# Optimization experiments

Measured on AMD Instinct MI355X. Metric: run time of the kernel, lower is better.

## Reference

```python
import jax, jax.numpy as jnp
import numpy as np
import math

B, Q, K, C, H, D = 4, 2048, 2048, 128, 8, 16  # c_q=c_k=c_v=C, c_hidden=D, no_heads=H


def setup_inputs() -> dict:
    key = jax.random.key(0)
    k1, k2, k3, k4, k5 = jax.random.split(key, 5)
    return {
        "q_x": jax.random.normal(k1, (B, Q, C), dtype=jnp.float32),
        "kv_x": jax.random.normal(k2, (B, K, C), dtype=jnp.float32),
        # torch Linear weight layout [out_features, in_features] = [H*D, C]
        "w_q": jax.random.normal(k3, (H * D, C), dtype=jnp.float32) * (1.0 / math.sqrt(C)),
        "w_k": jax.random.normal(k4, (H * D, C), dtype=jnp.float32) * (1.0 / math.sqrt(C)),
        "w_v": jax.random.normal(k5, (H * D, C), dtype=jnp.float32) * (1.0 / math.sqrt(C)),
    }


def reference(q_x, kv_x, w_q, w_k, w_v):
    # project + split heads: [B, S, C] x [H, D, C] -> [B, H, S, D]
    wq = w_q.reshape(H, D, C)
    wk = w_k.reshape(H, D, C)
    wv = w_v.reshape(H, D, C)
    q = jnp.einsum("bqc,hdc->bhqd", q_x, wq) / math.sqrt(D)
    k = jnp.einsum("bkc,hdc->bhkd", kv_x, wk)
    v = jnp.einsum("bkc,hdc->bhkd", kv_x, wv)
    scores = jnp.einsum("bhqd,bhkd->bhqk", q, k)  # [B, H, Q, K]
    a = jax.nn.softmax(scores, axis=-1)
    o = jnp.einsum("bhqk,bhkd->bqhd", a, v)  # transpose(-2,-3) -> [B, Q, H, D]
    return o
```

## Files before the change

kernel.cpp:

```cpp
#include <hip/hip_runtime.h>

constexpr int NB   = 4;
constexpr int SEQ  = 2048;
constexpr int CDIM = 128;
constexpr int NH   = 8;
constexpr int HD   = 16;

typedef _Float16 h_t;
typedef __attribute__((ext_vector_type(4))) _Float16 h4;
typedef __attribute__((ext_vector_type(8))) _Float16 h8;
typedef __attribute__((ext_vector_type(2))) __fp16   fp2;
typedef __attribute__((ext_vector_type(4))) float    f4;

constexpr float LOG2E = 1.44269504f;
constexpr float BIAS  = -8.0f * LOG2E;

__global__ __launch_bounds__(256)
void proj(const float* __restrict__ qx, const float* __restrict__ kvx,
          const float* __restrict__ wq, const float* __restrict__ wk,
          const float* __restrict__ wv,
          h_t* __restrict__ qh, h_t* __restrict__ kh, h_t* __restrict__ vF)
{
    const int mat = blockIdx.y;
    const int mb  = blockIdx.x * 64;
    const int wv_ = threadIdx.x >> 6;
    const int ln  = threadIdx.x & 63;
    const int r   = ln & 15, kg = ln >> 4;
    const int row = mb + wv_ * 16 + r;

    const float* x = (mat == 0) ? qx : kvx;
    const float* w = (mat == 0) ? wq : (mat == 1) ? wk : wv;
    h_t*         o = (mat == 0) ? qh : (mat == 1) ? kh : vF;
    const float xs = (mat == 0) ? 0.25f * LOG2E : 1.0f;

    h8 a[4];
    #pragma unroll
    for (int kc = 0; kc < 4; ++kc) {
        const float* xp = x + (size_t)row * CDIM + kc * 32 + kg * 8;
        f4 x0 = *(const f4*)xp;
        f4 x1 = *(const f4*)(xp + 4);
        h8 tf;
        #pragma unroll
        for (int i = 0; i < 4; ++i) {
            tf[i]     = (h_t)(x0[i] * xs);
            tf[4 + i] = (h_t)(x1[i] * xs);
        }
        a[kc] = tf;
    }

    #pragma unroll
    for (int nt = 0; nt < 8; ++nt) {
        f4 acc = {0.f, 0.f, 0.f, 0.f};
        #pragma unroll
        for (int kc = 0; kc < 4; ++kc) {
            const float* wp = w + (size_t)(nt * 16 + r) * CDIM + kc * 32 + kg * 8;
            f4 w0 = *(const f4*)wp;
            f4 w1 = *(const f4*)(wp + 4);
            h8 b;
            #pragma unroll
            for (int i = 0; i < 4; ++i) { b[i] = (h_t)w0[i]; b[4 + i] = (h_t)w1[i]; }
            acc = __builtin_amdgcn_mfma_f32_16x16x32_f16(a[kc], b, acc, 0, 0, 0);
        }
        #pragma unroll
        for (int reg = 0; reg < 4; ++reg) {
            const int gr = mb + wv_ * 16 + 4 * kg + reg;
            const int b_ = gr >> 11, s = gr & (SEQ - 1);
            if (mat == 2)
                o[(((size_t)b_ * NH + nt) * 128 + (s >> 4)) * 256 + r * 16 + (s & 15)]
                    = (h_t)acc[reg];
            else
                o[(((size_t)b_ * NH + nt) * SEQ + s) * HD + r] = (h_t)acc[reg];
        }
    }
}

__global__ __launch_bounds__(256)
void attn(const h_t* __restrict__ qh, const h_t* __restrict__ kh,
          const h_t* __restrict__ vF, float* __restrict__ out)
{
    const int bh  = blockIdx.y;
    const int wv_ = threadIdx.x >> 6;
    const int ln  = threadIdx.x & 63;
    const int r   = ln & 15, kg = ln >> 4;

    const size_t hb = (size_t)bh * SEQ * HD;
    const int qb = blockIdx.x * 64 + wv_ * 16;

    h4 qf = *(const h4*)(qh + hb + (size_t)(qb + r) * HD + kg * 4);

    const h_t* kp = kh + hb + r * HD + kg * 4;
    const h_t* vp = vF + hb + r * 16 + kg * 4;

    float la = 0.f, lb = 0.f;
    f4 o = {0.f, 0.f, 0.f, 0.f};
    const f4 cbias = {BIAS, BIAS, BIAS, BIAS};

    h4 kfa = *(const h4*)(kp);
    h4 vfa = *(const h4*)(vp);
    h4 kfb = *(const h4*)(kp + 256);
    h4 vfb = *(const h4*)(vp + 256);

    for (int c = 0; c < SEQ / 16; c += 2) {
        h4 kfn0 = *(const h4*)(kp + (c + 2) * 256);
        h4 vfn0 = *(const h4*)(vp + (c + 2) * 256);
        h4 kfn1 = *(const h4*)(kp + (c + 3) * 256);
        h4 vfn1 = *(const h4*)(vp + (c + 3) * 256);

        {
            f4 s = __builtin_amdgcn_mfma_f32_16x16x16f16(kfa, qf, cbias, 0, 0, 0);
            const float e0 = __builtin_amdgcn_exp2f(s[0]);
            const float e1 = __builtin_amdgcn_exp2f(s[1]);
            const float e2 = __builtin_amdgcn_exp2f(s[2]);
            const float e3 = __builtin_amdgcn_exp2f(s[3]);
            la += e0 + e1; lb += e2 + e3;
            union { fp2 cc[2]; h4 v; } p;
            p.cc[0] = __builtin_amdgcn_cvt_pkrtz(e0, e1);
            p.cc[1] = __builtin_amdgcn_cvt_pkrtz(e2, e3);
            o = __builtin_amdgcn_mfma_f32_16x16x16f16(p.v, vfa, o, 0, 0, 0);
        }
        {
            f4 s = __builtin_amdgcn_mfma_f32_16x16x16f16(kfb, qf, cbias, 0, 0, 0);
            const float e0 = __builtin_amdgcn_exp2f(s[0]);
            const float e1 = __builtin_amdgcn_exp2f(s[1]);
            const float e2 = __builtin_amdgcn_exp2f(s[2]);
            const float e3 = __builtin_amdgcn_exp2f(s[3]);
            la += e0 + e1; lb += e2 + e3;
            union { fp2 cc[2]; h4 v; } p;
            p.cc[0] = __builtin_amdgcn_cvt_pkrtz(e0, e1);
            p.cc[1] = __builtin_amdgcn_cvt_pkrtz(e2, e3);
            o = __builtin_amdgcn_mfma_f32_16x16x16f16(p.v, vfb, o, 0, 0, 0);
        }

        kfa = kfn0; vfa = vfn0;
        kfb = kfn1; vfb = vfn1;
    }

    float l = la + lb;
    l += __shfl_xor(l, 16);
    l += __shfl_xor(l, 32);
    const float inv = 1.f / l;

    const int b_ = bh >> 3, h = bh & 7;
    #pragma unroll
    for (int reg = 0; reg < 4; ++reg) {
        const float iv = __shfl(inv, 4 * kg + reg);
        const int q = qb + 4 * kg + reg;
        out[(((size_t)b_ * SEQ + q) * NH + h) * HD + r] = o[reg] * iv;
    }
}

extern "C" void kernel_launch(void* const* d_in, const int* in_sizes, int n_in,
                              void* d_out, int out_size, void* d_ws, size_t ws_size,
                              hipStream_t stream) {
    const float* qx  = (const float*)d_in[0];
    const float* kvx = (const float*)d_in[1];
    const float* wq  = (const float*)d_in[2];
    const float* wk  = (const float*)d_in[3];
    const float* wv  = (const float*)d_in[4];
    float* out = (float*)d_out;

    h_t* qp = (h_t*)d_ws;
    h_t* kp = qp + (size_t)NB * NH * SEQ * HD;
    h_t* vp = kp + (size_t)NB * NH * SEQ * HD;

    proj<<<dim3(128, 3), dim3(256), 0, stream>>>(qx, kvx, wq, wk, wv, qp, kp, vp);
    attn<<<dim3(32, 32), dim3(256), 0, stream>>>(qp, kp, vp, out);
}
```

Baseline: 114.2 us.

## Process two query tiles per wave and split the key range into independent halves

Each wave now handles 32 queries (two 16-row tiles) instead of 16, so every K/V fragment it loads is reused for both tiles. The key sequence is split into a low and a high half, processed in the same loop iteration, which gives four independent MFMA/exp2 chains per iteration for more instruction-level parallelism. The partial sums and outputs of the two halves are combined at the end. The grid is halved to 512 blocks, which lowers the number of resident waves and raises register pressure. The prefetch at the end of the high half reads past the current head's data, but those values are never used.

```diff
diff --git a/kernel.cpp b/kernel.cpp
--- a/kernel.cpp
+++ b/kernel.cpp
@@ -74,6 +74,21 @@
     }
 }
 
+__device__ __forceinline__ void step(const h4& kf, const h4& vf, const h4& qf,
+                                     const f4& cbias, float& l, f4& o)
+{
+    f4 s = __builtin_amdgcn_mfma_f32_16x16x16f16(kf, qf, cbias, 0, 0, 0);
+    const float e0 = __builtin_amdgcn_exp2f(s[0]);
+    const float e1 = __builtin_amdgcn_exp2f(s[1]);
+    const float e2 = __builtin_amdgcn_exp2f(s[2]);
+    const float e3 = __builtin_amdgcn_exp2f(s[3]);
+    l += (e0 + e1) + (e2 + e3);
+    union { fp2 cc[2]; h4 v; } p;
+    p.cc[0] = __builtin_amdgcn_cvt_pkrtz(e0, e1);
+    p.cc[1] = __builtin_amdgcn_cvt_pkrtz(e2, e3);
+    o = __builtin_amdgcn_mfma_f32_16x16x16f16(p.v, vf, o, 0, 0, 0);
+}
+
 __global__ __launch_bounds__(256)
 void attn(const h_t* __restrict__ qh, const h_t* __restrict__ kh,
           const h_t* __restrict__ vF, float* __restrict__ out)
@@ -84,68 +99,59 @@
     const int r   = ln & 15, kg = ln >> 4;
 
     const size_t hb = (size_t)bh * SEQ * HD;
-    const int qb = blockIdx.x * 64 + wv_ * 16;
+    const int qb = blockIdx.x * 128 + wv_ * 32;
 
-    h4 qf = *(const h4*)(qh + hb + (size_t)(qb + r) * HD + kg * 4);
+    h4 qf0 = *(const h4*)(qh + hb + (size_t)(qb + r)      * HD + kg * 4);
+    h4 qf1 = *(const h4*)(qh + hb + (size_t)(qb + 16 + r) * HD + kg * 4);
 
     const h_t* kp = kh + hb + r * HD + kg * 4;
     const h_t* vp = vF + hb + r * 16 + kg * 4;
+    constexpr int HOF = 64 * 256;
 
-    float la = 0.f, lb = 0.f;
-    f4 o = {0.f, 0.f, 0.f, 0.f};
+    float l0L = 0.f, l0H = 0.f, l1L = 0.f, l1H = 0.f;
+    f4 o0L = {0.f, 0.f, 0.f, 0.f}, o0H = {0.f, 0.f, 0.f, 0.f};
+    f4 o1L = {0.f, 0.f, 0.f, 0.f}, o1H = {0.f, 0.f, 0.f, 0.f};
     const f4 cbias = {BIAS, BIAS, BIAS, BIAS};
 
-    h4 kfa = *(const h4*)(kp);
-    h4 vfa = *(const h4*)(vp);
-    h4 kfb = *(const h4*)(kp + 256);
-    h4 vfb = *(const h4*)(vp + 256);
+    h4 kLa = *(const h4*)(kp);             h4 vLa = *(const h4*)(vp);
+    h4 kHa = *(const h4*)(kp + HOF);       h4 vHa = *(const h4*)(vp + HOF);
+    h4 kLb = *(const h4*)(kp + 256);       h4 vLb = *(const h4*)(vp + 256);
+    h4 kHb = *(const h4*)(kp + HOF + 256); h4 vHb = *(const h4*)(vp + HOF + 256);
 
-    for (int c = 0; c < SEQ / 16; c += 2) {
-        h4 kfn0 = *(const h4*)(kp + (c + 2) * 256);
-        h4 vfn0 = *(const h4*)(vp + (c + 2) * 256);
-        h4 kfn1 = *(const h4*)(kp + (c + 3) * 256);
-        h4 vfn1 = *(const h4*)(vp + (c + 3) * 256);
+    for (int j = 0; j < 64; ++j) {
+        const int n = (j + 2) * 256;
+        h4 kLn = *(const h4*)(kp + n);
+        h4 vLn = *(const h4*)(vp + n);
+        h4 kHn = *(const h4*)(kp + HOF + n);
+        h4 vHn = *(const h4*)(vp + HOF + n);
 
-        {
-            f4 s = __builtin_amdgcn_mfma_f32_16x16x16f16(kfa, qf, cbias, 0, 0, 0);
-            const float e0 = __builtin_amdgcn_exp2f(s[0]);
-            const float e1 = __builtin_amdgcn_exp2f(s[1]);
-            const float e2 = __builtin_amdgcn_exp2f(s[2]);
-            const float e3 = __builtin_amdgcn_exp2f(s[3]);
-            la += e0 + e1; lb += e2 + e3;
-            union { fp2 cc[2]; h4 v; } p;
-            p.cc[0] = __builtin_amdgcn_cvt_pkrtz(e0, e1);
-            p.cc[1] = __builtin_amdgcn_cvt_pkrtz(e2, e3);
-            o = __builtin_amdgcn_mfma_f32_16x16x16f16(p.v, vfa, o, 0, 0, 0);
-        }
-        {
-            f4 s = __builtin_amdgcn_mfma_f32_16x16x16f16(kfb, qf, cbias, 0, 0, 0);
-            const float e0 = __builtin_amdgcn_exp2f(s[0]);
-            const float e1 = __builtin_amdgcn_exp2f(s[1]);
-            const float e2 = __builtin_amdgcn_exp2f(s[2]);
-            const float e3 = __builtin_amdgcn_exp2f(s[3]);
-            la += e0 + e1; lb += e2 + e3;
-            union { fp2 cc[2]; h4 v; } p;
-            p.cc[0] = __builtin_amdgcn_cvt_pkrtz(e0, e1);
-            p.cc[1] = __builtin_amdgcn_cvt_pkrtz(e2, e3);
-            o = __builtin_amdgcn_mfma_f32_16x16x16f16(p.v, vfb, o, 0, 0, 0);
-        }
+        step(kLa, vLa, qf0, cbias, l0L, o0L);
+        step(kHa, vHa, qf0, cbias, l0H, o0H);
+        step(kLa, vLa, qf1, cbias, l1L, o1L);
+        step(kHa, vHa, qf1, cbias, l1H, o1H);
 
-        kfa = kfn0; vfa = vfn0;
-        kfb = kfn1; vfb = vfn1;
+        kLa = kLb; vLa = vLb; kHa = kHb; vHa = vHb;
+        kLb = kLn; vLb = vLn; kHb = kHn; vHb = vHn;
     }
 
-    float l = la + lb;
-    l += __shfl_xor(l, 16);
-    l += __shfl_xor(l, 32);
-    const float inv = 1.f / l;
+    float l0 = l0L + l0H, l1 = l1L + l1H;
+    f4 o0, o1;
+    #pragma unroll
+    for (int i = 0; i < 4; ++i) { o0[i] = o0L[i] + o0H[i]; o1[i] = o1L[i] + o1H[i]; }
+
+    l0 += __shfl_xor(l0, 16); l0 += __shfl_xor(l0, 32);
+    l1 += __shfl_xor(l1, 16); l1 += __shfl_xor(l1, 32);
+    const float i0 = 1.f / l0, i1 = 1.f / l1;
 
     const int b_ = bh >> 3, h = bh & 7;
     #pragma unroll
     for (int reg = 0; reg < 4; ++reg) {
-        const float iv = __shfl(inv, 4 * kg + reg);
-        const int q = qb + 4 * kg + reg;
-        out[(((size_t)b_ * SEQ + q) * NH + h) * HD + r] = o[reg] * iv;
+        const float v0 = __shfl(i0, 4 * kg + reg);
+        const float v1 = __shfl(i1, 4 * kg + reg);
+        const int q0 = qb + 4 * kg + reg;
+        const int q1 = q0 + 16;
+        out[(((size_t)b_ * SEQ + q0) * NH + h) * HD + r] = o0[reg] * v0;
+        out[(((size_t)b_ * SEQ + q1) * NH + h) * HD + r] = o1[reg] * v1;
     }
 }
 
@@ -159,10 +165,11 @@
     const float* wv  = (const float*)d_in[4];
     float* out = (float*)d_out;
 
+    const size_t per = (size_t)NB * NH * SEQ * HD;
     h_t* qp = (h_t*)d_ws;
-    h_t* kp = qp + (size_t)NB * NH * SEQ * HD;
-    h_t* vp = kp + (size_t)NB * NH * SEQ * HD;
+    h_t* kp = qp + per;
+    h_t* vp = kp + per;
 
     proj<<<dim3(128, 3), dim3(256), 0, stream>>>(qx, kvx, wq, wk, wv, qp, kp, vp);
-    attn<<<dim3(32, 32), dim3(256), 0, stream>>>(qp, kp, vp, out);
+    attn<<<dim3(16, 32), dim3(256), 0, stream>>>(qp, kp, vp, out);
 }
```

Measured after the change: 116.8 us. +2.3%, slower.

## Split attention KV range across two wave groups and merge partials via LDS

Applied to the files above, without the earlier changes.

Doubles the attention block to 512 threads, where two groups of four waves each process half of the key/value sequence for the same query tile. Partial outputs and row sums from the second half are written to shared memory and combined by the first group before normalisation and store. This halves the serial KV loop per wave to raise latency hiding and occupancy, at the cost of a block barrier and an LDS reduction. Because no running max is tracked (a fixed bias is used), partials can be summed directly.

```diff
diff --git a/kernel.cpp b/kernel.cpp
--- a/kernel.cpp
+++ b/kernel.cpp
@@ -74,24 +74,29 @@
     }
 }
 
-__global__ __launch_bounds__(256)
+__global__ __launch_bounds__(512, 8)
 void attn(const h_t* __restrict__ qh, const h_t* __restrict__ kh,
           const h_t* __restrict__ vF, float* __restrict__ out)
 {
     const int bh  = blockIdx.y;
-    const int wv_ = threadIdx.x >> 6;
+    const int w   = threadIdx.x >> 6;
+    const int ws  = w & 3;
+    const int kvh = w >> 2;
     const int ln  = threadIdx.x & 63;
     const int r   = ln & 15, kg = ln >> 4;
 
+    __shared__ float oL[4][16][17];
+    __shared__ float lL[4][16];
+
     const size_t hb = (size_t)bh * SEQ * HD;
-    const int qb = blockIdx.x * 64 + wv_ * 16;
+    const int qb = blockIdx.x * 64 + ws * 16;
 
     h4 qf = *(const h4*)(qh + hb + (size_t)(qb + r) * HD + kg * 4);
 
-    const h_t* kp = kh + hb + r * HD + kg * 4;
-    const h_t* vp = vF + hb + r * 16 + kg * 4;
+    const h_t* kp = kh + hb + kvh * 64 * 256 + r * HD + kg * 4;
+    const h_t* vp = vF + hb + kvh * 64 * 256 + r * 16 + kg * 4;
 
-    float la = 0.f, lb = 0.f;
+    float l = 0.f;
     f4 o = {0.f, 0.f, 0.f, 0.f};
     const f4 cbias = {BIAS, BIAS, BIAS, BIAS};
 
@@ -100,7 +105,7 @@
     h4 kfb = *(const h4*)(kp + 256);
     h4 vfb = *(const h4*)(vp + 256);
 
-    for (int c = 0; c < SEQ / 16; c += 2) {
+    for (int c = 0; c < 64; c += 2) {
         h4 kfn0 = *(const h4*)(kp + (c + 2) * 256);
         h4 vfn0 = *(const h4*)(vp + (c + 2) * 256);
         h4 kfn1 = *(const h4*)(kp + (c + 3) * 256);
@@ -112,7 +117,7 @@
             const float e1 = __builtin_amdgcn_exp2f(s[1]);
             const float e2 = __builtin_amdgcn_exp2f(s[2]);
             const float e3 = __builtin_amdgcn_exp2f(s[3]);
-            la += e0 + e1; lb += e2 + e3;
+            l += (e0 + e1) + (e2 + e3);
             union { fp2 cc[2]; h4 v; } p;
             p.cc[0] = __builtin_amdgcn_cvt_pkrtz(e0, e1);
             p.cc[1] = __builtin_amdgcn_cvt_pkrtz(e2, e3);
@@ -124,7 +129,7 @@
             const float e1 = __builtin_amdgcn_exp2f(s[1]);
             const float e2 = __builtin_amdgcn_exp2f(s[2]);
             const float e3 = __builtin_amdgcn_exp2f(s[3]);
-            la += e0 + e1; lb += e2 + e3;
+            l += (e0 + e1) + (e2 + e3);
             union { fp2 cc[2]; h4 v; } p;
             p.cc[0] = __builtin_amdgcn_cvt_pkrtz(e0, e1);
             p.cc[1] = __builtin_amdgcn_cvt_pkrtz(e2, e3);
@@ -135,17 +140,31 @@
         kfb = kfn1; vfb = vfn1;
     }
 
-    float l = la + lb;
     l += __shfl_xor(l, 16);
     l += __shfl_xor(l, 32);
-    const float inv = 1.f / l;
 
-    const int b_ = bh >> 3, h = bh & 7;
-    #pragma unroll
-    for (int reg = 0; reg < 4; ++reg) {
-        const float iv = __shfl(inv, 4 * kg + reg);
-        const int q = qb + 4 * kg + reg;
-        out[(((size_t)b_ * SEQ + q) * NH + h) * HD + r] = o[reg] * iv;
+    if (kvh == 1) {
+        #pragma unroll
+        for (int reg = 0; reg < 4; ++reg)
+            oL[ws][4 * kg + reg][r] = o[reg];
+        if (ln < 16) lL[ws][r] = l;
+    }
+    __syncthreads();
+
+    if (kvh == 0) {
+        #pragma unroll
+        for (int reg = 0; reg < 4; ++reg)
+            o[reg] += oL[ws][4 * kg + reg][r];
+        l += lL[ws][r];
+        const float inv = 1.f / l;
+
+        const int b_ = bh >> 3, h = bh & 7;
+        #pragma unroll
+        for (int reg = 0; reg < 4; ++reg) {
+            const float iv = __shfl(inv, 4 * kg + reg);
+            const int q = qb + 4 * kg + reg;
+            out[(((size_t)b_ * SEQ + q) * NH + h) * HD + r] = o[reg] * iv;
+        }
     }
 }
 
@@ -159,10 +178,11 @@
     const float* wv  = (const float*)d_in[4];
     float* out = (float*)d_out;
 
+    const size_t per = (size_t)NB * NH * SEQ * HD;
     h_t* qp = (h_t*)d_ws;
-    h_t* kp = qp + (size_t)NB * NH * SEQ * HD;
-    h_t* vp = kp + (size_t)NB * NH * SEQ * HD;
+    h_t* kp = qp + per;
+    h_t* vp = kp + per;
 
     proj<<<dim3(128, 3), dim3(256), 0, stream>>>(qx, kvx, wq, wk, wv, qp, kp, vp);
-    attn<<<dim3(32, 32), dim3(256), 0, stream>>>(qp, kp, vp, out);
+    attn<<<dim3(32, 32), dim3(512), 0, stream>>>(qp, kp, vp, out);
 }
```

Result: no change. 115.2 us (+0.9%).
